# Kernel optimization log

Hardware: AMD Instinct MI355X
Metric: run time of the kernel (lower is better)

## Reference

```python
import jax, jax.numpy as jnp
import numpy as np
import math

N, T, D, H = 64, 512, 1024, 1024

def setup_inputs() -> dict:
    key = jax.random.key(0)
    k1, k2, k3, k4 = jax.random.split(key, 4)
    x = jax.random.normal(k1, (N, T, D), dtype=jnp.float32)
    h0 = jax.random.normal(k2, (N, H), dtype=jnp.float32)
    Wx = jax.random.normal(k3, (D, 4 * H), dtype=jnp.float32) / math.sqrt(D)
    Wh = jax.random.normal(k4, (H, 4 * H), dtype=jnp.float32) / math.sqrt(H)
    b = jnp.zeros((4 * H,), dtype=jnp.float32)
    return {"x": x, "h0": h0, "Wx": Wx, "Wh": Wh, "b": b}

def reference(x, h0, Wx, Wh, b):
    Hdim = h0.shape[1]
    c0 = jnp.zeros_like(h0)
    # Precompute input projection for all timesteps: [N,T,4H] -> time-major [T,N,4H]
    xW = jnp.einsum('ntd,dk->tnk', x, Wx) + b

    def step(carry, xw_t):
        prev_h, prev_c = carry
        a = xw_t + prev_h @ Wh  # [N, 4H]
        i = jax.nn.sigmoid(a[:, :Hdim])
        f = jax.nn.sigmoid(a[:, Hdim:2 * Hdim])
        o = jax.nn.sigmoid(a[:, 2 * Hdim:3 * Hdim])
        g = jnp.tanh(a[:, 3 * Hdim:])
        next_c = f * prev_c + i * g
        next_h = o * jnp.tanh(next_c)
        return (next_h, next_c), next_h

    _, hs = jax.lax.scan(step, (h0, c0), xW)  # hs: [T, N, H]
    return jnp.transpose(hs, (1, 0, 2))  # [N, T, H]
```

## Files before the change

kernel.cpp:

```cpp
#include <hip/hip_runtime.h>

typedef short bf16x8 __attribute__((ext_vector_type(8)));
typedef float f32x4 __attribute__((ext_vector_type(4)));

static constexpr int kT = 512;
static constexpr int kN = 64;
static constexpr int kD = 1024;
static constexpr int kH = 1024;
static constexpr int kG = 4 * kH;

__device__ __forceinline__ unsigned short f2bf(float f) {
  unsigned u = __builtin_bit_cast(unsigned, f);
  return (unsigned short)((u + 0x7fffu + ((u >> 16) & 1u)) >> 16);
}
__device__ __forceinline__ unsigned pack2(float a, float b) {
  return (unsigned)f2bf(a) | ((unsigned)f2bf(b) << 16);
}
__device__ __forceinline__ float fsigmoid(float v) {
  return __builtin_amdgcn_rcpf(1.0f + __expf(-v));
}
__device__ __forceinline__ float ftanh(float v) {
  return 1.0f - 2.0f * __builtin_amdgcn_rcpf(__expf(2.0f * v) + 1.0f);
}

__device__ __forceinline__ bf16x8 gld16_coh(unsigned long long a) {
  bf16x8 r;
  asm volatile("global_load_dwordx4 %0, %1, off sc0 sc1" : "=v"(r) : "v"(a) : "memory");
  return r;
}
__device__ __forceinline__ bf16x8 gld16(unsigned long long a) {
  bf16x8 r;
  asm volatile("global_load_dwordx4 %0, %1, off" : "=v"(r) : "v"(a) : "memory");
  return r;
}

#define VMCNT(n) do { asm volatile("s_waitcnt vmcnt(" #n ")" ::: "memory"); \
                      __builtin_amdgcn_sched_barrier(0); } while (0)

__global__ __launch_bounds__(256) void xconv(const float* __restrict__ x,
                                             unsigned short* __restrict__ xbf) {
  const int gid = blockIdx.x * 256 + threadIdx.x;
  const float4* x4 = (const float4*)x;
  uint4* o = (uint4*)xbf;
  for (int i = gid; i < (kN * kT * kD) / 8; i += 2048 * 256) {
    const float4 f0 = x4[2 * i];
    const float4 f1 = x4[2 * i + 1];
    uint4 p;
    p.x = pack2(f0.x, f0.y); p.y = pack2(f0.z, f0.w);
    p.z = pack2(f1.x, f1.y); p.w = pack2(f1.z, f1.w);
    o[i] = p;
  }
}

template <bool PRE>
__global__ __launch_bounds__(256, 1)
void lstm_fg(const float* __restrict__ x, const float* __restrict__ h0,
             const float* __restrict__ Wx, const float* __restrict__ Wh,
             const float* __restrict__ bias, float* __restrict__ out,
             unsigned short* __restrict__ hbuf, unsigned* __restrict__ flags,
             const unsigned short* __restrict__ xbf) {
  __shared__ float ps[2][16 * 320];

  const int tid = threadIdx.x;
  const int bx = blockIdx.x;
  const int dom = (bx & 7) >> 1;
  const int ug = ((bx >> 3) << 1) | (bx & 1);
  const int wv = tid >> 6;
  const int lane = tid & 63;

  const int colc = ug * 16 + (lane & 15);
  const int krow = (lane >> 4) * 8;
  const int kb = wv * 256;
  bf16x8 wxf[4][8], whf[4][8];
#pragma unroll
  for (int ct = 0; ct < 4; ++ct) {
#pragma unroll
    for (int ks = 0; ks < 8; ++ks) {
      bf16x8 vx, vh;
#pragma unroll
      for (int e = 0; e < 8; ++e) {
        const size_t k = (size_t)(kb + ks * 32 + krow + e);
        vx[e] = (short)f2bf(Wx[k * kG + ct * kH + colc]);
        vh[e] = (short)f2bf(Wh[k * kG + ct * kH + colc]);
      }
      wxf[ct][ks] = vx;
      whf[ct][ks] = vh;
    }
  }

  const int n_l = tid >> 4;
  const int j_l = tid & 15;
  const int jg = ug * 16 + j_l;
  const float b_i = bias[jg];
  const float b_f = bias[kH + jg];
  const float b_o = bias[2 * kH + jg];
  const float b_g = bias[3 * kH + jg];
  float c = 0.0f;

  const int arow = lane & 15;
  const int nrow = dom * 16 + arow;
  const unsigned long long xbase0 =
      (unsigned long long)nrow * kT * kD * 2 + (unsigned long long)(kb + krow) * 2;
  const unsigned long long hbase0 =
      (unsigned long long)nrow * kH * 2 + (unsigned long long)(kb + krow) * 2;
  const unsigned pubeidx = (unsigned)((dom * 16 + n_l) * kH + jg);

  unsigned* myflag = flags + (dom * 256 + ug * 4 + wv);
  unsigned* pollp = flags + (dom * 256 + wv * 64 + lane);

  bf16x8 xfrag[8], hfrag[8];

  if (PRE) {
    const unsigned long long xb = (unsigned long long)xbf + xbase0;
#pragma unroll
    for (int ks = 0; ks < 8; ++ks) xfrag[ks] = gld16(xb + (unsigned)(ks * 64));
    VMCNT(0);
  } else {
    const float* xr = x + (size_t)nrow * kT * kD + (kb + krow);
#pragma unroll
    for (int ks = 0; ks < 8; ++ks) {
      const float4 f0 = *(const float4*)(xr + ks * 32);
      const float4 f1 = *(const float4*)(xr + ks * 32 + 4);
      bf16x8 v;
      v[0] = (short)f2bf(f0.x); v[1] = (short)f2bf(f0.y);
      v[2] = (short)f2bf(f0.z); v[3] = (short)f2bf(f0.w);
      v[4] = (short)f2bf(f1.x); v[5] = (short)f2bf(f1.y);
      v[6] = (short)f2bf(f1.z); v[7] = (short)f2bf(f1.w);
      xfrag[ks] = v;
    }
  }
  f32x4 acc[4];
#pragma unroll
  for (int ct = 0; ct < 4; ++ct) acc[ct] = (f32x4){0.f, 0.f, 0.f, 0.f};
#pragma unroll
  for (int ks = 0; ks < 8; ++ks)
#pragma unroll
    for (int ct = 0; ct < 4; ++ct)
      acc[ct] = __builtin_amdgcn_mfma_f32_16x16x32_bf16(xfrag[ks], wxf[ct][ks], acc[ct], 0, 0, 0);
  {
    const float* hr = h0 + (size_t)nrow * kH + (kb + krow);
#pragma unroll
    for (int ks = 0; ks < 8; ++ks) {
      const float4 f0 = *(const float4*)(hr + ks * 32);
      const float4 f1 = *(const float4*)(hr + ks * 32 + 4);
      bf16x8 v;
      v[0] = (short)f2bf(f0.x); v[1] = (short)f2bf(f0.y);
      v[2] = (short)f2bf(f0.z); v[3] = (short)f2bf(f0.w);
      v[4] = (short)f2bf(f1.x); v[5] = (short)f2bf(f1.y);
      v[6] = (short)f2bf(f1.z); v[7] = (short)f2bf(f1.w);
      hfrag[ks] = v;
    }
  }
  VMCNT(0);

  for (int t = 0; t < kT; ++t) {
    VMCNT(4);
    __builtin_amdgcn_sched_barrier(0);
#pragma unroll
    for (int ks = 0; ks < 4; ++ks)
#pragma unroll
      for (int ct = 0; ct < 4; ++ct)
        acc[ct] = __builtin_amdgcn_mfma_f32_16x16x32_bf16(hfrag[ks], whf[ct][ks], acc[ct], 0, 0, 0);
    VMCNT(0);
#pragma unroll
    for (int ks = 4; ks < 8; ++ks)
#pragma unroll
      for (int ct = 0; ct < 4; ++ct)
        acc[ct] = __builtin_amdgcn_mfma_f32_16x16x32_bf16(hfrag[ks], whf[ct][ks], acc[ct], 0, 0, 0);

    float* p = ps[t & 1];
#pragma unroll
    for (int ct = 0; ct < 4; ++ct)
      *(f32x4*)&p[(ct * 4 + wv) * 320 + (lane & 15) * 20 + (lane >> 4) * 4] = acc[ct];
    __syncthreads();

    float a4[4];
#pragma unroll
    for (int g = 0; g < 4; ++g) {
      a4[g] = p[(g * 4 + 0) * 320 + j_l * 20 + n_l]
            + p[(g * 4 + 1) * 320 + j_l * 20 + n_l]
            + p[(g * 4 + 2) * 320 + j_l * 20 + n_l]
            + p[(g * 4 + 3) * 320 + j_l * 20 + n_l];
    }
    const float gi = fsigmoid(a4[0] + b_i);
    const float gf = fsigmoid(a4[1] + b_f);
    const float go = fsigmoid(a4[2] + b_o);
    const float gg = ftanh(a4[3] + b_g);
    c = gf * c + gi * gg;
    const float hv = go * ftanh(c);

    if (t < kT - 1) {
      const unsigned tgt = (unsigned)(t + 1);
      const unsigned buf1 = tgt & 1;
      const unsigned mybf = (unsigned)f2bf(hv);
      const unsigned up = (unsigned)__shfl_xor((int)mybf, 1);

      if (PRE) {
        if ((j_l & 1) == 0) {
          __hip_atomic_store((unsigned*)(hbuf + buf1 * (kN * kH) + pubeidx),
                             mybf | (up << 16), __ATOMIC_RELAXED, __HIP_MEMORY_SCOPE_AGENT);
        }
        const unsigned long long xb = (unsigned long long)xbf + xbase0 +
                                      (unsigned long long)(t + 1) * 2048u;
#pragma unroll
        for (int ks = 0; ks < 8; ++ks) xfrag[ks] = gld16(xb + (unsigned)(ks * 64));
        VMCNT(8);
        if (lane == 0)
          __hip_atomic_store(myflag, tgt, __ATOMIC_RELAXED, __HIP_MEMORY_SCOPE_AGENT);
        VMCNT(0);
      } else {
        if ((j_l & 1) == 0) {
          __hip_atomic_store((unsigned*)(hbuf + buf1 * (kN * kH) + pubeidx),
                             mybf | (up << 16), __ATOMIC_RELAXED, __HIP_MEMORY_SCOPE_AGENT);
        }
        VMCNT(0);
        if (lane == 0)
          __hip_atomic_store(myflag, tgt, __ATOMIC_RELAXED, __HIP_MEMORY_SCOPE_AGENT);
        const float* xr = x + (size_t)nrow * kT * kD + (size_t)(t + 1) * kD + (kb + krow);
#pragma unroll
        for (int ks = 0; ks < 8; ++ks) {
          const float4 f0 = *(const float4*)(xr + ks * 32);
          const float4 f1 = *(const float4*)(xr + ks * 32 + 4);
          bf16x8 v;
          v[0] = (short)f2bf(f0.x); v[1] = (short)f2bf(f0.y);
          v[2] = (short)f2bf(f0.z); v[3] = (short)f2bf(f0.w);
          v[4] = (short)f2bf(f1.x); v[5] = (short)f2bf(f1.y);
          v[6] = (short)f2bf(f1.z); v[7] = (short)f2bf(f1.w);
          xfrag[ks] = v;
        }
      }

#pragma unroll
      for (int ct = 0; ct < 4; ++ct) acc[ct] = (f32x4){0.f, 0.f, 0.f, 0.f};
#pragma unroll
      for (int ks = 0; ks < 8; ++ks)
#pragma unroll
        for (int ct = 0; ct < 4; ++ct)
          acc[ct] = __builtin_amdgcn_mfma_f32_16x16x32_bf16(xfrag[ks], wxf[ct][ks], acc[ct], 0, 0, 0);

      __builtin_amdgcn_sched_barrier(0);
      __builtin_nontemporal_store(hv, &out[((size_t)(dom * 16 + n_l) * kT + t) * kH + jg]);

      for (;;) {
        const unsigned v = __hip_atomic_load(pollp, __ATOMIC_RELAXED,
                                             __HIP_MEMORY_SCOPE_AGENT);
        if (__all((int)v >= (int)tgt)) break;
        __builtin_amdgcn_s_sleep(1);
      }
      __builtin_amdgcn_sched_barrier(0);

      const unsigned long long hb = (unsigned long long)hbuf +
                                    (unsigned long long)buf1 * (kN * kH * 2) + hbase0;
#pragma unroll
      for (int ks = 0; ks < 8; ++ks) hfrag[ks] = gld16_coh(hb + (unsigned)(ks * 64));
    } else {
      __builtin_nontemporal_store(hv, &out[((size_t)(dom * 16 + n_l) * kT + t) * kH + jg]);
    }
  }
}

extern "C" void kernel_launch(void* const* d_in, const int* in_sizes, int n_in,
                              void* d_out, int out_size, void* d_ws, size_t ws_size,
                              hipStream_t stream) {
  (void)in_sizes; (void)n_in; (void)out_size;
  const float* x  = (const float*)d_in[0];
  const float* h0 = (const float*)d_in[1];
  const float* Wx = (const float*)d_in[2];
  const float* Wh = (const float*)d_in[3];
  const float* b  = (const float*)d_in[4];
  float* out = (float*)d_out;

  const size_t o_hbuf = 4096;
  const size_t o_xbf = o_hbuf + 262144;
  const size_t need_pre = o_xbf + (size_t)kN * kT * kD * 2;

  unsigned* flags = (unsigned*)d_ws;
  unsigned short* hbuf = (unsigned short*)((char*)d_ws + o_hbuf);
  unsigned short* xbf = (unsigned short*)((char*)d_ws + o_xbf);

  hipMemsetAsync(d_ws, 0, 4096, stream);

  if (ws_size >= need_pre) {
    hipLaunchKernelGGL(xconv, dim3(2048), dim3(256), 0, stream, x, xbf);
    hipLaunchKernelGGL(HIP_KERNEL_NAME(lstm_fg<true>), dim3(256), dim3(256), 0, stream,
                       x, h0, Wx, Wh, b, out, hbuf, flags, xbf);
  } else {
    hipLaunchKernelGGL(HIP_KERNEL_NAME(lstm_fg<false>), dim3(256), dim3(256), 0, stream,
                       x, h0, Wx, Wh, b, out, hbuf, flags,
                       (const unsigned short*)nullptr);
  }
}
```

Measured before the change: 2.043 ms.

## Aggregate per-wave flags into one per-workgroup flag with single-wave polling

Each wave now bumps a shared-memory counter, and the fourth wave to arrive publishes a single per-workgroup global flag, which cuts the flag array from 256 to 64 entries per domain. Only wave 0 polls the global flags and then releases the other waves through an LDS variable, so the other three waves spin on LDS instead. The aim is less L2 polling traffic and fewer flag loads per step. The cost is an extra serialization hop through LDS, and the LDS variables are initialized without a barrier before first use, which relies on the existing per-step __syncthreads for ordering.

New measurement: 1.991 ms. 2.5% less time.

```diff
diff --git a/kernel.cpp b/kernel.cpp
--- a/kernel.cpp
+++ b/kernel.cpp
@@ -54,12 +54,14 @@
 
 template <bool PRE>
 __global__ __launch_bounds__(256, 1)
-void lstm_fg(const float* __restrict__ x, const float* __restrict__ h0,
-             const float* __restrict__ Wx, const float* __restrict__ Wh,
-             const float* __restrict__ bias, float* __restrict__ out,
-             unsigned short* __restrict__ hbuf, unsigned* __restrict__ flags,
-             const unsigned short* __restrict__ xbf) {
+void lstm_fg3(const float* __restrict__ x, const float* __restrict__ h0,
+              const float* __restrict__ Wx, const float* __restrict__ Wh,
+              const float* __restrict__ bias, float* __restrict__ out,
+              unsigned short* __restrict__ hbuf, unsigned* __restrict__ flags,
+              const unsigned short* __restrict__ xbf) {
   __shared__ float ps[2][16 * 320];
+  __shared__ unsigned wgcnt;
+  __shared__ unsigned rel;
 
   const int tid = threadIdx.x;
   const int bx = blockIdx.x;
@@ -67,6 +69,8 @@
   const int ug = ((bx >> 3) << 1) | (bx & 1);
   const int wv = tid >> 6;
   const int lane = tid & 63;
+
+  if (tid == 0) { wgcnt = 0u; rel = 0u; }
 
   const int colc = ug * 16 + (lane & 15);
   const int krow = (lane >> 4) * 8;
@@ -105,8 +109,8 @@
       (unsigned long long)nrow * kH * 2 + (unsigned long long)(kb + krow) * 2;
   const unsigned pubeidx = (unsigned)((dom * 16 + n_l) * kH + jg);
 
-  unsigned* myflag = flags + (dom * 256 + ug * 4 + wv);
-  unsigned* pollp = flags + (dom * 256 + wv * 64 + lane);
+  unsigned* myflag = flags + (dom * 64 + ug);
+  unsigned* pollp = flags + (dom * 64 + lane);
 
   bf16x8 xfrag[8], hfrag[8];
 
@@ -155,7 +159,6 @@
 
   for (int t = 0; t < kT; ++t) {
     VMCNT(4);
-    __builtin_amdgcn_sched_barrier(0);
 #pragma unroll
     for (int ks = 0; ks < 4; ++ks)
 #pragma unroll
@@ -205,8 +208,11 @@
 #pragma unroll
         for (int ks = 0; ks < 8; ++ks) xfrag[ks] = gld16(xb + (unsigned)(ks * 64));
         VMCNT(8);
-        if (lane == 0)
-          __hip_atomic_store(myflag, tgt, __ATOMIC_RELAXED, __HIP_MEMORY_SCOPE_AGENT);
+        if (lane == 0) {
+          const unsigned old = atomicAdd(&wgcnt, 1u);
+          if (old == 4u * (unsigned)t + 3u)
+            __hip_atomic_store(myflag, tgt, __ATOMIC_RELAXED, __HIP_MEMORY_SCOPE_AGENT);
+        }
         VMCNT(0);
       } else {
         if ((j_l & 1) == 0) {
@@ -214,8 +220,11 @@
                              mybf | (up << 16), __ATOMIC_RELAXED, __HIP_MEMORY_SCOPE_AGENT);
         }
         VMCNT(0);
-        if (lane == 0)
-          __hip_atomic_store(myflag, tgt, __ATOMIC_RELAXED, __HIP_MEMORY_SCOPE_AGENT);
+        if (lane == 0) {
+          const unsigned old = atomicAdd(&wgcnt, 1u);
+          if (old == 4u * (unsigned)t + 3u)
+            __hip_atomic_store(myflag, tgt, __ATOMIC_RELAXED, __HIP_MEMORY_SCOPE_AGENT);
+        }
         const float* xr = x + (size_t)nrow * kT * kD + (size_t)(t + 1) * kD + (kb + krow);
 #pragma unroll
         for (int ks = 0; ks < 8; ++ks) {
@@ -241,11 +250,17 @@
       __builtin_amdgcn_sched_barrier(0);
       __builtin_nontemporal_store(hv, &out[((size_t)(dom * 16 + n_l) * kT + t) * kH + jg]);
 
-      for (;;) {
-        const unsigned v = __hip_atomic_load(pollp, __ATOMIC_RELAXED,
-                                             __HIP_MEMORY_SCOPE_AGENT);
-        if (__all((int)v >= (int)tgt)) break;
-        __builtin_amdgcn_s_sleep(1);
+      if (wv == 0) {
+        for (;;) {
+          const unsigned v = __hip_atomic_load(pollp, __ATOMIC_RELAXED,
+                                               __HIP_MEMORY_SCOPE_AGENT);
+          if (__all((int)v >= (int)tgt)) break;
+          __builtin_amdgcn_s_sleep(1);
+        }
+        __hip_atomic_store(&rel, tgt, __ATOMIC_RELAXED, __HIP_MEMORY_SCOPE_WORKGROUP);
+      } else {
+        while (__hip_atomic_load(&rel, __ATOMIC_RELAXED, __HIP_MEMORY_SCOPE_WORKGROUP) < tgt)
+          __builtin_amdgcn_s_sleep(1);
       }
       __builtin_amdgcn_sched_barrier(0);
 
@@ -282,10 +297,10 @@
 
   if (ws_size >= need_pre) {
     hipLaunchKernelGGL(xconv, dim3(2048), dim3(256), 0, stream, x, xbf);
-    hipLaunchKernelGGL(HIP_KERNEL_NAME(lstm_fg<true>), dim3(256), dim3(256), 0, stream,
+    hipLaunchKernelGGL(HIP_KERNEL_NAME(lstm_fg3<true>), dim3(256), dim3(256), 0, stream,
                        x, h0, Wx, Wh, b, out, hbuf, flags, xbf);
   } else {
-    hipLaunchKernelGGL(HIP_KERNEL_NAME(lstm_fg<false>), dim3(256), dim3(256), 0, stream,
+    hipLaunchKernelGGL(HIP_KERNEL_NAME(lstm_fg3<false>), dim3(256), dim3(256), 0, stream,
                        x, h0, Wx, Wh, b, out, hbuf, flags,
                        (const unsigned short*)nullptr);
   }
```
